# Kernel optimization log

Measured on AMD Instinct MI355X. Metric: run time of the kernel, lower is better.

The kernel has to match this reference:

```python
import jax, jax.numpy as jnp
import numpy as np

HEADS = 8
DIM = 512
DIM_HEAD = DIM // 8        # 64
M = DIM // 2               # 256 landmarks
PINV_ITERS = 6
KERNEL = 33                # residual depthwise conv kernel (33,1)


def moore_penrose_pinv(x, iters):
    # x: [b, h, m, m]; Newton-Schulz style iterative pseudoinverse (lucidrains impl)
    abs_x = jnp.abs(x)
    col = abs_x.sum(axis=-1)
    row = abs_x.sum(axis=-2)
    z = jnp.swapaxes(x, -1, -2) / (jnp.max(col) * jnp.max(row))
    I = jnp.eye(x.shape[-1], dtype=x.dtype)
    for _ in range(iters):
        xz = x @ z
        z = 0.25 * z @ (13.0 * I - xz @ (15.0 * I - xz @ (7.0 * I - xz)))
    return z


def setup_inputs() -> dict:
    key = jax.random.key(0)
    ks = jax.random.split(key, 5)
    b, n, dim = 4, 8192, DIM
    x = jax.random.normal(ks[0], (b, n, dim), dtype=jnp.float32)
    # to_qkv: Linear(dim, 3*inner_dim, bias=False); inner_dim = heads*dim_head = dim
    w_qkv = jax.random.normal(ks[1], (dim, 3 * dim), dtype=jnp.float32) / np.sqrt(dim)
    # to_out: Linear(inner_dim, dim) with bias (dropout = identity in eval)
    w_out = jax.random.normal(ks[2], (dim, dim), dtype=jnp.float32) / np.sqrt(dim)
    b_out = jax.random.normal(ks[3], (dim,), dtype=jnp.float32) * 0.01
    # res_conv: Conv2d(heads, heads, (33,1), padding=(16,0), groups=heads, bias=False)
    conv_w = jax.random.normal(ks[4], (HEADS, 1, KERNEL, 1), dtype=jnp.float32) / np.sqrt(KERNEL)
    return {"x": x, "w_qkv": w_qkv, "w_out": w_out, "b_out": b_out, "conv_w": conv_w}


def nystrom_attention(x, w_qkv, w_out, b_out, conv_w):
    b, n, dim = x.shape
    h, d, m = HEADS, DIM_HEAD, M
    # pad front so seq len divisible by num_landmarks (no-op for n=8192, m=256)
    pad = (m - n % m) % m
    xp = jnp.pad(x, ((0, 0), (pad, 0), (0, 0)))
    np_ = n + pad

    qkv = xp @ w_qkv                                   # [b, np, 3*dim]
    q, k, v = jnp.split(qkv, 3, axis=-1)
    to_heads = lambda t: t.reshape(b, np_, h, d).transpose(0, 2, 1, 3)  # [b,h,np,d]
    q, k, v = to_heads(q), to_heads(k), to_heads(v)
    q = q * (d ** -0.5)

    l = np_ // m                                       # tokens per landmark
    pool = lambda t: t.reshape(b, h, m, l, d).mean(axis=3)  # [b,h,m,d]
    q_l, k_l = pool(q), pool(k)

    attn1 = jax.nn.softmax(jnp.einsum('bhnd,bhmd->bhnm', q, k_l), axis=-1)    # [b,h,np,m]
    attn2 = jax.nn.softmax(jnp.einsum('bhid,bhjd->bhij', q_l, k_l), axis=-1)  # [b,h,m,m]
    attn3 = jax.nn.softmax(jnp.einsum('bhmd,bhnd->bhmn', q_l, k), axis=-1)    # [b,h,m,np]

    attn2_inv = moore_penrose_pinv(attn2, PINV_ITERS)
    out = (attn1 @ attn2_inv) @ (attn3 @ v)            # [b,h,np,d]

    # depthwise conv residual over the sequence axis, per head
    res = jax.lax.conv_general_dilated(
        v, conv_w, window_strides=(1, 1),
        padding=((KERNEL // 2, KERNEL // 2), (0, 0)),
        dimension_numbers=('NCHW', 'OIHW', 'NCHW'),
        feature_group_count=h)
    out = out + res

    out = out.transpose(0, 2, 1, 3).reshape(b, np_, dim)
    out = out @ w_out + b_out
    return out[:, -n:]


def reference(x, w_qkv, w_out, b_out, conv_w):
    return x + nystrom_attention(x, w_qkv, w_out, b_out, conv_w)
```

## Files before the change

kernel.cpp:

```cpp
#include <hip/hip_runtime.h>


#define N_SEQ 8192
#define DMODEL 512
#define NHEAD 8
#define DHEAD 64
#define NLAND 256
#define BH 32

typedef unsigned short u16;
typedef __attribute__((ext_vector_type(8))) short bh8;
typedef __attribute__((ext_vector_type(4))) float fx4;

__device__ __forceinline__ float bf2f(u16 u) { return __uint_as_float(((unsigned)u) << 16); }
__device__ __forceinline__ u16 f2bf(float f) {
    unsigned x = __float_as_uint(f);
    return (u16)((x + 0x7fffu + ((x >> 16) & 1u)) >> 16);
}
__device__ __forceinline__ fx4 mfma16(bh8 a, bh8 b, fx4 c) {
    return __builtin_amdgcn_mfma_f32_16x16x32_bf16(a, b, c, 0, 0, 0);
}
__device__ __forceinline__ void gload16(u16* lds, const u16* g) {
    __builtin_amdgcn_global_load_lds(
        (const __attribute__((address_space(1))) unsigned int*)g,
        (__attribute__((address_space(3))) unsigned int*)lds, 16, 0, 0);
}

__global__ void detect_kernel(const u16* __restrict__ X, unsigned* flag_out)
{
    __shared__ int cnt;
    if (threadIdx.x == 0) cnt = 0;
    __syncthreads();
    u16 u = X[threadIdx.x * 2];
    int e = (u >> 7) & 0xFF;
    int insane = (u != 0) && (e < 90 || e > 140);
    atomicAdd(&cnt, insane);
    __syncthreads();
    if (threadIdx.x == 0) flag_out[0] = (cnt > 64) ? 1u : 0u;
}

__global__ __launch_bounds__(256) void convert4_kernel(
    const void* __restrict__ in, u16* __restrict__ out, int n4, const unsigned* __restrict__ flag)
{
    int i = blockIdx.x * 256 + threadIdx.x;
    if (i >= n4) return;
    if (flag[0]) {
        float4 v = ((const float4*)in)[i];
        ushort4 o;
        o.x = f2bf(v.x); o.y = f2bf(v.y); o.z = f2bf(v.z); o.w = f2bf(v.w);
        ((ushort4*)out)[i] = o;
    } else {
        ((ushort4*)out)[i] = ((const ushort4*)in)[i];
    }
}

__global__ __launch_bounds__(256) void wtrans_kernel(
    const void* __restrict__ in, u16* __restrict__ out, int rows, int cols,
    const unsigned* __restrict__ flag)
{
    int idx = blockIdx.x * 256 + threadIdx.x;
    if (idx >= rows * cols) return;
    int r = idx / cols, c = idx % cols;
    float v = flag[0] ? ((const float*)in)[idx] : bf2f(((const u16*)in)[idx]);
    out[(size_t)c * rows + r] = f2bf(v);
}

__global__ __launch_bounds__(256) void qkv_mfma_kernel(
    const u16* __restrict__ X, const u16* __restrict__ WT,
    u16* __restrict__ Q, u16* __restrict__ K, u16* __restrict__ VT)
{
    __shared__ u16 Xs[128 * 64];
    __shared__ u16 Ws[128 * 64];
    const int tid = threadIdx.x;
    const int wave = tid >> 6, lane = tid & 63;
    const int wrow = (wave >> 1) * 64, wcol = (wave & 1) * 64;
    const int i0 = blockIdx.x * 128;
    const int j0 = blockIdx.y * 128;
    const int la = lane >> 3, lb = lane & 7;
    const int lm = lane & 15, lq = lane >> 4;
    const int sw = lm & 7;
    const int sc = (lb ^ la) * 8;
    fx4 acc[4][4];
#pragma unroll
    for (int a = 0; a < 4; ++a)
#pragma unroll
        for (int b = 0; b < 4; ++b) acc[a][b] = (fx4){0.f, 0.f, 0.f, 0.f};

    for (int k0 = 0; k0 < DMODEL; k0 += 64) {
        __syncthreads();
#pragma unroll
        for (int jj = 0; jj < 4; ++jj) {
            int rb = wave * 32 + jj * 8;
            gload16(Xs + rb * 64, X + (size_t)(i0 + rb + la) * DMODEL + k0 + sc);
            gload16(Ws + rb * 64, WT + (size_t)(j0 + rb + la) * DMODEL + k0 + sc);
        }
        __syncthreads();
#pragma unroll
        for (int ks = 0; ks < 2; ++ks) {
            const int po = ((ks * 4 + lq) ^ sw) * 8;
            bh8 xf[4], wf[4];
#pragma unroll
            for (int im = 0; im < 4; ++im)
                xf[im] = *(const bh8*)(Xs + (wrow + im * 16 + lm) * 64 + po);
#pragma unroll
            for (int in = 0; in < 4; ++in)
                wf[in] = *(const bh8*)(Ws + (wcol + in * 16 + lm) * 64 + po);
#pragma unroll
            for (int im = 0; im < 4; ++im)
#pragma unroll
                for (int in = 0; in < 4; ++in)
                    acc[im][in] = mfma16(wf[in], xf[im], acc[im][in]);
        }
    }
#pragma unroll
    for (int im = 0; im < 4; ++im) {
        int m = i0 + wrow + im * 16 + lm;
        int bb = m >> 13, ns = m & (N_SEQ - 1);
#pragma unroll
        for (int in = 0; in < 4; ++in) {
            int nn = j0 + wcol + in * 16 + (lq << 2);
            int which = nn >> 9;
            int h = (nn >> 6) & 7;
            int d = nn & 63;
            if (which == 2) {
                size_t vb = (size_t)(bb * NHEAD + h) * DHEAD;
#pragma unroll
                for (int cc = 0; cc < 4; ++cc)
                    VT[(vb + d + cc) * N_SEQ + ns] = f2bf(acc[im][in][cc]);
            } else {
                u16* dst = (which == 0) ? Q : K;
                float s = (which == 0) ? 0.125f : 1.f;
                ushort4 o;
                o.x = f2bf(acc[im][in][0] * s); o.y = f2bf(acc[im][in][1] * s);
                o.z = f2bf(acc[im][in][2] * s); o.w = f2bf(acc[im][in][3] * s);
                *(ushort4*)(dst + ((size_t)(bb * NHEAD + h) * N_SEQ + ns) * DHEAD + d) = o;
            }
        }
    }
}

__global__ __launch_bounds__(64) void pool_kernel(
    const u16* __restrict__ Q, const u16* __restrict__ K,
    float* __restrict__ QL, float* __restrict__ KL,
    u16* __restrict__ QLb, u16* __restrict__ KLb)
{
    int m = blockIdx.x, bh = blockIdx.y, d = threadIdx.x;
    size_t base = ((size_t)bh * N_SEQ + m * 32) * DHEAD + d;
    float sq = 0.f, sk = 0.f;
#pragma unroll
    for (int i = 0; i < 32; ++i) {
        sq += bf2f(Q[base + i * DHEAD]);
        sk += bf2f(K[base + i * DHEAD]);
    }
    size_t ob = ((size_t)bh * NLAND + m) * DHEAD + d;
    sq *= (1.f / 32.f); sk *= (1.f / 32.f);
    QL[ob] = sq; KL[ob] = sk;
    QLb[ob] = f2bf(sq); KLb[ob] = f2bf(sk);
}

__global__ __launch_bounds__(256) void attn2_kernel(
    const float* __restrict__ QL, const float* __restrict__ KL, float* __restrict__ A2)
{
    __shared__ float qrow[64];
    __shared__ float red[256];
    int i = blockIdx.x, bh = blockIdx.y, j = threadIdx.x;
    if (j < 64) qrow[j] = QL[((size_t)bh * NLAND + i) * DHEAD + j];
    __syncthreads();
    const float* kr = KL + ((size_t)bh * NLAND + j) * DHEAD;
    float lg = 0.f;
#pragma unroll
    for (int d = 0; d < 64; ++d) lg += qrow[d] * kr[d];
    red[j] = lg; __syncthreads();
    for (int s = 128; s > 0; s >>= 1) { if (j < s) red[j] = fmaxf(red[j], red[j + s]); __syncthreads(); }
    float mx = red[0]; __syncthreads();
    float p = __expf(lg - mx);
    red[j] = p; __syncthreads();
    for (int s = 128; s > 0; s >>= 1) { if (j < s) red[j] += red[j + s]; __syncthreads(); }
    float sum = red[0];
    A2[((size_t)bh * NLAND + i) * NLAND + j] = p / sum;
}

__global__ void init_scal_kernel(unsigned* scal) { if (threadIdx.x < 2) scal[threadIdx.x] = 0u; }

__global__ __launch_bounds__(256) void absmax_kernel(const float* __restrict__ A2, unsigned* scal)
{
    __shared__ float red[256];
    int bh = blockIdx.x, t = threadIdx.x;
    const float* Ab = A2 + (size_t)bh * 65536;
    float cs = 0.f, rs = 0.f;
    for (int j = 0; j < 256; ++j) cs += fabsf(Ab[t * 256 + j]);
    for (int i = 0; i < 256; ++i) rs += fabsf(Ab[i * 256 + t]);
    red[t] = cs; __syncthreads();
    for (int s = 128; s > 0; s >>= 1) { if (t < s) red[t] = fmaxf(red[t], red[t + s]); __syncthreads(); }
    if (t == 0) atomicMax(scal + 0, __float_as_uint(red[0]));
    __syncthreads();
    red[t] = rs; __syncthreads();
    for (int s = 128; s > 0; s >>= 1) { if (t < s) red[t] = fmaxf(red[t], red[t + s]); __syncthreads(); }
    if (t == 0) atomicMax(scal + 1, __float_as_uint(red[0]));
}

__global__ __launch_bounds__(256) void z0_kernel(
    const float* __restrict__ A2, const unsigned* __restrict__ scal,
    u16* __restrict__ zb, u16* __restrict__ zbT, u16* __restrict__ A2b)
{
    float inv = 1.f / (__uint_as_float(scal[0]) * __uint_as_float(scal[1]));
    size_t idx = (size_t)blockIdx.x * 256 + threadIdx.x;
    size_t bh = idx >> 16;
    int r = (int)(idx & 65535);
    int i = r >> 8, j = r & 255;
    float a = A2[idx];
    zb[idx]  = f2bf(A2[(bh << 16) + (size_t)j * 256 + i] * inv);
    zbT[idx] = f2bf(a * inv);
    A2b[idx] = f2bf(a);
}

__global__ __launch_bounds__(256) void bgemm_mfma_kernel(
    const u16* __restrict__ A, const u16* __restrict__ BT,
    u16* __restrict__ Cn, u16* __restrict__ Ct, const u16* __restrict__ E,
    int N, long sB, long sCn, long sCt, float sc, float alpha, float beta, int wn, int wt)
{
    __shared__ u16 As[64 * 72];
    __shared__ u16 Bs[64 * 72];
    const int tid = threadIdx.x;
    const int wave = tid >> 6, lane = tid & 63;
    const int wm = (wave >> 1) * 32, wnn = (wave & 1) * 32;
    const int i0 = blockIdx.x * 64, j0 = blockIdx.y * 64, bh = blockIdx.z;
    const u16* Ab = A + (size_t)bh * 65536;
    const u16* Bb = BT + (size_t)bh * sB;
    const int srow = tid >> 2, scol = (tid & 3) * 16;
    const int lm = lane & 15, lq = lane >> 4;
    fx4 acc[2][2];
#pragma unroll
    for (int a = 0; a < 2; ++a)
#pragma unroll
        for (int b = 0; b < 2; ++b) acc[a][b] = (fx4){0.f, 0.f, 0.f, 0.f};

    for (int k0 = 0; k0 < 256; k0 += 64) {
        uint4 a0 = *(const uint4*)(Ab + (size_t)(i0 + srow) * 256 + k0 + scol);
        uint4 a1 = *(const uint4*)(Ab + (size_t)(i0 + srow) * 256 + k0 + scol + 8);
        uint4 b0 = *(const uint4*)(Bb + (size_t)(j0 + srow) * 256 + k0 + scol);
        uint4 b1 = *(const uint4*)(Bb + (size_t)(j0 + srow) * 256 + k0 + scol + 8);
        __syncthreads();
        *(uint4*)(As + srow * 72 + scol) = a0;
        *(uint4*)(As + srow * 72 + scol + 8) = a1;
        *(uint4*)(Bs + srow * 72 + scol) = b0;
        *(uint4*)(Bs + srow * 72 + scol + 8) = b1;
        __syncthreads();
#pragma unroll
        for (int ks = 0; ks < 2; ++ks) {
            bh8 lf[2], rf[2];
#pragma unroll
            for (int im = 0; im < 2; ++im)
                lf[im] = *(const bh8*)(As + (wm + im * 16 + lm) * 72 + ks * 32 + lq * 8);
#pragma unroll
            for (int in = 0; in < 2; ++in)
                rf[in] = *(const bh8*)(Bs + (wnn + in * 16 + lm) * 72 + ks * 32 + lq * 8);
#pragma unroll
            for (int im = 0; im < 2; ++im)
#pragma unroll
                for (int in = 0; in < 2; ++in)
                    acc[im][in] = mfma16(lf[im], rf[in], acc[im][in]);
        }
    }
#pragma unroll
    for (int im = 0; im < 2; ++im) {
#pragma unroll
        for (int in = 0; in < 2; ++in) {
            int n = j0 + wnn + in * 16 + lm;
            int m0 = i0 + wm + im * 16 + (lq << 2);
            float c[4];
#pragma unroll
            for (int r = 0; r < 4; ++r) {
                int m = m0 + r;
                float x = beta * acc[im][in][r];
                if (alpha != 0.f)
                    x += alpha * bf2f(E[(size_t)bh * 65536 + (size_t)m * 256 + n]);
                if (m == n) x += sc;
                c[r] = x;
            }
            if (wn) {
#pragma unroll
                for (int r = 0; r < 4; ++r)
                    Cn[(size_t)bh * sCn + (size_t)(m0 + r) * N + n] = f2bf(c[r]);
            }
            if (wt) {
                ushort4 o;
                o.x = f2bf(c[0]); o.y = f2bf(c[1]); o.z = f2bf(c[2]); o.w = f2bf(c[3]);
                *(ushort4*)(Ct + (size_t)bh * sCt + (size_t)n * 256 + m0) = o;
            }
        }
    }
}

__global__ __launch_bounds__(256, 2) void attn3v_mfma_kernel(
    const u16* __restrict__ QLb, const u16* __restrict__ Kb,
    const u16* __restrict__ VTb, u16* __restrict__ PO, float* __restrict__ ML)
{
    __shared__ u16 Ks[64 * 72];
    __shared__ u16 Vs[64 * 72];
    __shared__ u16 Pw[4][64 * 72];
    const int tid = threadIdx.x;
    const int wave = tid >> 6, lane = tid & 63;
    const int q = lane >> 4, l15 = lane & 15;
    const int part = blockIdx.x;
    const int bh = blockIdx.y;
    const int nbase = part * 512;
    const int srow = tid >> 2, scol = (tid & 3) * 16;
    u16* Pp = Pw[wave];
    bh8 qf[4][2];
#pragma unroll
    for (int mt = 0; mt < 4; ++mt)
#pragma unroll
        for (int ks = 0; ks < 2; ++ks)
            qf[mt][ks] = *(const bh8*)(QLb + ((size_t)bh * NLAND + wave * 64 + mt * 16 + l15) * DHEAD + ks * 32 + q * 8);
    float M[4] = {-1e30f, -1e30f, -1e30f, -1e30f};
    float L[4] = {0.f, 0.f, 0.f, 0.f};
    fx4 O[4][4];
#pragma unroll
    for (int mt = 0; mt < 4; ++mt)
#pragma unroll
        for (int dt = 0; dt < 4; ++dt) O[mt][dt] = (fx4){0.f, 0.f, 0.f, 0.f};

    for (int c = 0; c < 8; ++c) {
        const int n0 = nbase + c * 64;
        uint4 k0v = *(const uint4*)(Kb + ((size_t)bh * N_SEQ + n0 + srow) * DHEAD + scol);
        uint4 k1v = *(const uint4*)(Kb + ((size_t)bh * N_SEQ + n0 + srow) * DHEAD + scol + 8);
        uint4 v0v = *(const uint4*)(VTb + ((size_t)bh * DHEAD + srow) * N_SEQ + n0 + scol);
        uint4 v1v = *(const uint4*)(VTb + ((size_t)bh * DHEAD + srow) * N_SEQ + n0 + scol + 8);
        __syncthreads();
        *(uint4*)(Ks + srow * 72 + scol) = k0v;
        *(uint4*)(Ks + srow * 72 + scol + 8) = k1v;
        *(uint4*)(Vs + srow * 72 + scol) = v0v;
        *(uint4*)(Vs + srow * 72 + scol + 8) = v1v;
        __syncthreads();
        fx4 S[4][4];
#pragma unroll
        for (int nt = 0; nt < 4; ++nt)
#pragma unroll
            for (int mt = 0; mt < 4; ++mt) S[nt][mt] = (fx4){0.f, 0.f, 0.f, 0.f};
#pragma unroll
        for (int ks = 0; ks < 2; ++ks) {
            bh8 kf[4];
#pragma unroll
            for (int nt = 0; nt < 4; ++nt)
                kf[nt] = *(const bh8*)(Ks + (nt * 16 + l15) * 72 + ks * 32 + q * 8);
#pragma unroll
            for (int nt = 0; nt < 4; ++nt)
#pragma unroll
                for (int mt = 0; mt < 4; ++mt)
                    S[nt][mt] = mfma16(kf[nt], qf[mt][ks], S[nt][mt]);
        }
#pragma unroll
        for (int mt = 0; mt < 4; ++mt) {
            float cm = -1e30f;
#pragma unroll
            for (int nt = 0; nt < 4; ++nt)
#pragma unroll
                for (int r = 0; r < 4; ++r) cm = fmaxf(cm, S[nt][mt][r]);
            cm = fmaxf(cm, __shfl_xor(cm, 16));
            cm = fmaxf(cm, __shfl_xor(cm, 32));
            float Mn = fmaxf(M[mt], cm);
            float al = __expf(M[mt] - Mn);
            M[mt] = Mn;
            L[mt] *= al;
#pragma unroll
            for (int dt = 0; dt < 4; ++dt) {
                O[mt][dt][0] *= al; O[mt][dt][1] *= al;
                O[mt][dt][2] *= al; O[mt][dt][3] *= al;
            }
            float ps = 0.f;
#pragma unroll
            for (int nt = 0; nt < 4; ++nt)
#pragma unroll
                for (int r = 0; r < 4; ++r) {
                    float p = __expf(S[nt][mt][r] - Mn);
                    ps += p;
                    Pp[(mt * 16 + l15) * 72 + nt * 16 + q * 4 + r] = f2bf(p);
                }
            ps += __shfl_xor(ps, 16);
            ps += __shfl_xor(ps, 32);
            L[mt] += ps;
        }
#pragma unroll
        for (int ks = 0; ks < 2; ++ks) {
            bh8 pf[4];
#pragma unroll
            for (int mt = 0; mt < 4; ++mt)
                pf[mt] = *(const bh8*)(Pp + (mt * 16 + l15) * 72 + ks * 32 + q * 8);
#pragma unroll
            for (int dt = 0; dt < 4; ++dt) {
                bh8 vf = *(const bh8*)(Vs + (dt * 16 + l15) * 72 + ks * 32 + q * 8);
#pragma unroll
                for (int mt = 0; mt < 4; ++mt)
                    O[mt][dt] = mfma16(vf, pf[mt], O[mt][dt]);
            }
        }
    }
#pragma unroll
    for (int mt = 0; mt < 4; ++mt) {
        size_t mrow = (size_t)(bh * 16 + part) * NLAND + wave * 64 + mt * 16 + l15;
#pragma unroll
        for (int dt = 0; dt < 4; ++dt) {
            ushort4 o;
            o.x = f2bf(O[mt][dt][0]); o.y = f2bf(O[mt][dt][1]);
            o.z = f2bf(O[mt][dt][2]); o.w = f2bf(O[mt][dt][3]);
            *(ushort4*)(PO + mrow * DHEAD + dt * 16 + q * 4) = o;
        }
        if (q == 0) { ML[mrow * 2] = M[mt]; ML[mrow * 2 + 1] = L[mt]; }
    }
}

__global__ __launch_bounds__(64) void combine_kernel(
    const u16* __restrict__ PO, const float* __restrict__ ML, u16* __restrict__ W3VT)
{
    int m = blockIdx.x, bh = blockIdx.y, d = threadIdx.x;
    float Mg = -1e30f;
#pragma unroll
    for (int p = 0; p < 16; ++p)
        Mg = fmaxf(Mg, ML[((size_t)(bh * 16 + p) * NLAND + m) * 2]);
    float denom = 0.f, o = 0.f;
#pragma unroll
    for (int p = 0; p < 16; ++p) {
        size_t ix = (size_t)(bh * 16 + p) * NLAND + m;
        float w = __expf(ML[ix * 2] - Mg);
        denom += ML[ix * 2 + 1] * w;
        o += bf2f(PO[ix * DHEAD + d]) * w;
    }
    W3VT[((size_t)bh * DHEAD + d) * NLAND + m] = f2bf(o / denom);
}

__global__ __launch_bounds__(256) void conv_kernel(
    const u16* __restrict__ VT, const u16* __restrict__ CW, u16* __restrict__ RT)
{
    __shared__ float vl[2080];
    __shared__ float cws[33];
    const int tid = threadIdx.x;
    const int c0 = blockIdx.x * 2048;
    const int row = blockIdx.y;
    const int h = (row >> 6) & 7;
    const u16* src = VT + (size_t)row * N_SEQ;
    for (int i = tid; i < 2080; i += 256) {
        int gn = c0 - 16 + i;
        vl[i] = (gn >= 0 && gn < N_SEQ) ? bf2f(src[gn]) : 0.f;
    }
    if (tid < 33) cws[tid] = bf2f(CW[h * 33 + tid]);
    __syncthreads();
    float v[40];
    const int base = tid * 8;
#pragma unroll
    for (int i = 0; i < 40; ++i) v[i] = vl[base + i];
    float s[8];
#pragma unroll
    for (int j = 0; j < 8; ++j) {
        float a = 0.f;
#pragma unroll
        for (int t = 0; t < 33; ++t) a += cws[t] * v[j + t];
        s[j] = a;
    }
    u16* dst = RT + (size_t)row * N_SEQ + c0 + base;
    ushort4 o0, o1;
    o0.x = f2bf(s[0]); o0.y = f2bf(s[1]); o0.z = f2bf(s[2]); o0.w = f2bf(s[3]);
    o1.x = f2bf(s[4]); o1.y = f2bf(s[5]); o1.z = f2bf(s[6]); o1.w = f2bf(s[7]);
    *(ushort4*)dst = o0;
    *(ushort4*)(dst + 4) = o1;
}

__global__ __launch_bounds__(256) void outheads_mfma_kernel(
    const u16* __restrict__ Qb, const u16* __restrict__ KLb,
    const u16* __restrict__ WMT, const u16* __restrict__ RT,
    u16* __restrict__ Y)
{
    __shared__ u16 Pl[64 * 264];
    __shared__ float wmax[4][64];
    __shared__ float wsum[4][64];
    const int tid = threadIdx.x;
    const int wave = tid >> 6, lane = tid & 63;
    const int q = lane >> 4, l15 = lane & 15;
    const int bh = blockIdx.y;
    const int bb = bh >> 3, h = bh & 7;
    const int n0 = blockIdx.x * 64;
    fx4 S[4][4];
#pragma unroll
    for (int a = 0; a < 4; ++a)
#pragma unroll
        for (int b = 0; b < 4; ++b) S[a][b] = (fx4){0.f, 0.f, 0.f, 0.f};
#pragma unroll
    for (int ks = 0; ks < 2; ++ks) {
        bh8 qfr[4];
#pragma unroll
        for (int nt = 0; nt < 4; ++nt)
            qfr[nt] = *(const bh8*)(Qb + ((size_t)bh * N_SEQ + n0 + nt * 16 + l15) * DHEAD + ks * 32 + q * 8);
#pragma unroll
        for (int mt = 0; mt < 4; ++mt) {
            bh8 kf = *(const bh8*)(KLb + ((size_t)bh * NLAND + wave * 64 + mt * 16 + l15) * DHEAD + ks * 32 + q * 8);
#pragma unroll
            for (int nt = 0; nt < 4; ++nt)
                S[nt][mt] = mfma16(qfr[nt], kf, S[nt][mt]);
        }
    }
#pragma unroll
    for (int nt = 0; nt < 4; ++nt)
#pragma unroll
        for (int r = 0; r < 4; ++r) {
            float pm = fmaxf(fmaxf(S[nt][0][r], S[nt][1][r]), fmaxf(S[nt][2][r], S[nt][3][r]));
            pm = fmaxf(pm, __shfl_xor(pm, 1));
            pm = fmaxf(pm, __shfl_xor(pm, 2));
            pm = fmaxf(pm, __shfl_xor(pm, 4));
            pm = fmaxf(pm, __shfl_xor(pm, 8));
            if (l15 == 0) wmax[wave][nt * 16 + q * 4 + r] = pm;
        }
    __syncthreads();
#pragma unroll
    for (int nt = 0; nt < 4; ++nt)
#pragma unroll
        for (int r = 0; r < 4; ++r) {
            int nl = nt * 16 + q * 4 + r;
            float Mf = fmaxf(fmaxf(wmax[0][nl], wmax[1][nl]), fmaxf(wmax[2][nl], wmax[3][nl]));
            float ps = 0.f;
#pragma unroll
            for (int mt = 0; mt < 4; ++mt) {
                float p = __expf(S[nt][mt][r] - Mf);
                ps += p;
                Pl[nl * 264 + wave * 64 + mt * 16 + l15] = f2bf(p);
            }
            ps += __shfl_xor(ps, 1);
            ps += __shfl_xor(ps, 2);
            ps += __shfl_xor(ps, 4);
            ps += __shfl_xor(ps, 8);
            if (l15 == 0) wsum[wave][nl] = ps;
        }
    __syncthreads();
    fx4 O[4];
#pragma unroll
    for (int nt = 0; nt < 4; ++nt) O[nt] = (fx4){0.f, 0.f, 0.f, 0.f};
#pragma unroll
    for (int ks = 0; ks < 8; ++ks) {
        bh8 af = *(const bh8*)(WMT + ((size_t)bh * DHEAD + wave * 16 + l15) * NLAND + ks * 32 + q * 8);
#pragma unroll
        for (int nt = 0; nt < 4; ++nt) {
            bh8 pf = *(const bh8*)(Pl + (size_t)(nt * 16 + l15) * 264 + ks * 32 + q * 8);
            O[nt] = mfma16(af, pf, O[nt]);
        }
    }
#pragma unroll
    for (int nt = 0; nt < 4; ++nt) {
        int nl = nt * 16 + l15;
        float inv = 1.f / (wsum[0][nl] + wsum[1][nl] + wsum[2][nl] + wsum[3][nl]);
        int d0 = wave * 16 + (q << 2);
        fx4 v = O[nt];
#pragma unroll
        for (int c = 0; c < 4; ++c)
            v[c] = v[c] * inv + bf2f(RT[(size_t)(bh * DHEAD + d0 + c) * N_SEQ + n0 + nl]);
        ushort4 o;
        o.x = f2bf(v[0]); o.y = f2bf(v[1]); o.z = f2bf(v[2]); o.w = f2bf(v[3]);
        *(ushort4*)(Y + ((size_t)bb * N_SEQ + n0 + nl) * DMODEL + h * DHEAD + d0) = o;
    }
}

__global__ __launch_bounds__(256) void final_mfma_kernel(
    const u16* __restrict__ Y, const u16* __restrict__ WT,
    const u16* __restrict__ Bias, const u16* __restrict__ X, void* __restrict__ Out,
    const unsigned* __restrict__ flag)
{
    __shared__ u16 Xs[128 * 64];
    __shared__ u16 Ws[128 * 64];
    const int tid = threadIdx.x;
    const int wave = tid >> 6, lane = tid & 63;
    const int wrow = (wave >> 1) * 64, wcol = (wave & 1) * 64;
    const int i0 = blockIdx.x * 128;
    const int j0 = blockIdx.y * 128;
    const int la = lane >> 3, lb = lane & 7;
    const int lm = lane & 15, lq = lane >> 4;
    const int sw = lm & 7;
    const int sc = (lb ^ la) * 8;
    const unsigned isf32 = flag[0];
    fx4 acc[4][4];
#pragma unroll
    for (int a = 0; a < 4; ++a)
#pragma unroll
        for (int b = 0; b < 4; ++b) acc[a][b] = (fx4){0.f, 0.f, 0.f, 0.f};

    for (int k0 = 0; k0 < DMODEL; k0 += 64) {
        __syncthreads();
#pragma unroll
        for (int jj = 0; jj < 4; ++jj) {
            int rb = wave * 32 + jj * 8;
            gload16(Xs + rb * 64, Y + (size_t)(i0 + rb + la) * DMODEL + k0 + sc);
            gload16(Ws + rb * 64, WT + (size_t)(j0 + rb + la) * DMODEL + k0 + sc);
        }
        __syncthreads();
#pragma unroll
        for (int ks = 0; ks < 2; ++ks) {
            const int po = ((ks * 4 + lq) ^ sw) * 8;
            bh8 xf[4], wf[4];
#pragma unroll
            for (int im = 0; im < 4; ++im)
                xf[im] = *(const bh8*)(Xs + (wrow + im * 16 + lm) * 64 + po);
#pragma unroll
            for (int in = 0; in < 4; ++in)
                wf[in] = *(const bh8*)(Ws + (wcol + in * 16 + lm) * 64 + po);
#pragma unroll
            for (int im = 0; im < 4; ++im)
#pragma unroll
                for (int in = 0; in < 4; ++in)
                    acc[im][in] = mfma16(wf[in], xf[im], acc[im][in]);
        }
    }
#pragma unroll
    for (int im = 0; im < 4; ++im) {
        int m = i0 + wrow + im * 16 + lm;
#pragma unroll
        for (int in = 0; in < 4; ++in) {
            int nn = j0 + wcol + in * 16 + (lq << 2);
            ushort4 b4 = *(const ushort4*)(Bias + nn);
            ushort4 x4 = *(const ushort4*)(X + (size_t)m * DMODEL + nn);
            float c0 = acc[im][in][0] + bf2f(b4.x) + bf2f(x4.x);
            float c1 = acc[im][in][1] + bf2f(b4.y) + bf2f(x4.y);
            float c2 = acc[im][in][2] + bf2f(b4.z) + bf2f(x4.z);
            float c3 = acc[im][in][3] + bf2f(b4.w) + bf2f(x4.w);
            if (isf32) {
                *(float4*)((float*)Out + (size_t)m * DMODEL + nn) = make_float4(c0, c1, c2, c3);
            } else {
                ushort4 o;
                o.x = f2bf(c0); o.y = f2bf(c1); o.z = f2bf(c2); o.w = f2bf(c3);
                *(ushort4*)((u16*)Out + (size_t)m * DMODEL + nn) = o;
            }
        }
    }
}

extern "C" void kernel_launch(void* const* d_in, const int* in_sizes, int n_in,
                              void* d_out, int out_size, void* d_ws, size_t ws_size,
                              hipStream_t stream)
{
    (void)in_sizes; (void)n_in; (void)out_size; (void)ws_size;
    char* ws = (char*)d_ws;
    u16*   Xc    = (u16*)(ws + 0);
    u16*   WqkvT = (u16*)(ws + 33554432);
    u16*   WoutT = (u16*)(ws + 35127296);
    u16*   Boutc = (u16*)(ws + 35651584);
    u16*   CWc   = (u16*)(ws + 35652608);
    u16*   Qb    = (u16*)(ws + 35653632);
    u16*   Kb    = (u16*)(ws + 69208064);
    u16*   RT    = (u16*)(ws + 69208064);
    u16*   VTb   = (u16*)(ws + 102762496);
    float* QL    = (float*)(ws + 136316928);
    float* KL    = (float*)(ws + 138414080);
    u16*   QLb   = (u16*)(ws + 140511232);
    u16*   KLb   = (u16*)(ws + 141559808);
    u16*   W3VT  = (u16*)(ws + 142608384);
    u16*   WMT   = (u16*)(ws + 143656960);
    u16*   A2b   = (u16*)(ws + 144705536);
    u16*   zA    = (u16*)(ws + 148899840);
    u16*   zAT   = (u16*)(ws + 153094144);
    float* A2    = (float*)(ws + 157288448);
    u16*   PO    = (u16*)(ws + 157288448);
    float* ML    = (float*)(ws + 174065664);
    u16*   zB    = (u16*)(ws + 165677056);
    u16*   zBT   = (u16*)(ws + 169871360);
    u16*   xz    = (u16*)(ws + 174065664);
    u16*   xzT   = (u16*)(ws + 178259968);
    u16*   t2T   = (u16*)(ws + 182454272);
    u16*   t3T   = (u16*)(ws + 186648576);
    u16*   Yb    = (u16*)(ws + 157288448);
    unsigned* SCAL = (unsigned*)(ws + 190842880);

    detect_kernel<<<1, 256, 0, stream>>>((const u16*)d_in[0], SCAL + 2);
    convert4_kernel<<<16384, 256, 0, stream>>>(d_in[0], Xc, 4194304, SCAL + 2);
    wtrans_kernel<<<3072, 256, 0, stream>>>(d_in[1], WqkvT, 512, 1536, SCAL + 2);
    wtrans_kernel<<<1024, 256, 0, stream>>>(d_in[2], WoutT, 512, 512, SCAL + 2);
    convert4_kernel<<<1, 256, 0, stream>>>(d_in[3], Boutc, 128, SCAL + 2);
    convert4_kernel<<<1, 256, 0, stream>>>(d_in[4], CWc, 66, SCAL + 2);

    qkv_mfma_kernel<<<dim3(256, 12), 256, 0, stream>>>(Xc, WqkvT, Qb, Kb, VTb);
    pool_kernel<<<dim3(256, BH), 64, 0, stream>>>(Qb, Kb, QL, KL, QLb, KLb);
    attn2_kernel<<<dim3(256, BH), 256, 0, stream>>>(QL, KL, A2);
    init_scal_kernel<<<1, 64, 0, stream>>>(SCAL);
    absmax_kernel<<<32, 256, 0, stream>>>(A2, SCAL);
    z0_kernel<<<8192, 256, 0, stream>>>(A2, SCAL, zA, zAT, A2b);

    attn3v_mfma_kernel<<<dim3(16, BH), 256, 0, stream>>>(QLb, Kb, VTb, PO, ML);
    combine_kernel<<<dim3(256, BH), 64, 0, stream>>>(PO, ML, W3VT);
    conv_kernel<<<dim3(4, 2048), 256, 0, stream>>>(VTb, CWc, RT);

    u16 *z = zA, *zT = zAT, *zn = zB, *znT = zBT;
    for (int it = 0; it < 6; ++it) {
        bgemm_mfma_kernel<<<dim3(4, 4, 32), 256, 0, stream>>>(
            A2b, zT, xz, xzT, A2b, 256, 65536, 65536, 65536, 0.f, 0.f, 1.f, 1, 1);
        bgemm_mfma_kernel<<<dim3(4, 4, 32), 256, 0, stream>>>(
            xz, xzT, xz, t2T, xz, 256, 65536, 65536, 65536, 15.f, -7.f, 1.f, 0, 1);
        bgemm_mfma_kernel<<<dim3(4, 4, 32), 256, 0, stream>>>(
            xz, t2T, xz, t3T, xz, 256, 65536, 65536, 65536, 13.f, 0.f, -1.f, 0, 1);
        bgemm_mfma_kernel<<<dim3(4, 4, 32), 256, 0, stream>>>(
            z, t3T, zn, znT, xz, 256, 65536, 65536, 65536, 0.f, 0.f, 0.25f, 1, 1);
        u16* t;
        t = z; z = zn; zn = t;
        t = zT; zT = znT; znT = t;
    }
    bgemm_mfma_kernel<<<dim3(4, 1, 32), 256, 0, stream>>>(
        z, W3VT, WMT, WMT, xz, 64, 16384, 16384, 16384, 0.f, 0.f, 1.f, 0, 1);
    outheads_mfma_kernel<<<dim3(128, BH), 256, 0, stream>>>(Qb, KLb, WMT, RT, Yb);
    final_mfma_kernel<<<dim3(256, 4), 256, 0, stream>>>(Yb, WoutT, Boutc, Xc, d_out, SCAL + 2);
}
```

Measured before the change: 732.5 us.

## Give each wave full landmark rows in outheads kernel to drop block syncs

The outheads kernel now has each wave own 16 query rows across all 256 landmarks, instead of splitting landmarks across waves. The softmax max and sum can then be reduced within a wave, which removes the cross-wave LDS reductions and both __syncthreads. The second MFMA swaps operand roles so the residual read is a vectorized ushort4 load, and launch bounds request 4 blocks per SIMD. In exchange each wave reads all of KL and WMT itself, and the output stores become scalar 2-byte writes.

```diff
diff --git a/kernel.cpp b/kernel.cpp
--- a/kernel.cpp
+++ b/kernel.cpp
@@ -465,95 +465,87 @@
     *(ushort4*)(dst + 4) = o1;
 }
 
-__global__ __launch_bounds__(256) void outheads_mfma_kernel(
+__global__ __launch_bounds__(256, 4) void outheads_mfma_kernel(
     const u16* __restrict__ Qb, const u16* __restrict__ KLb,
     const u16* __restrict__ WMT, const u16* __restrict__ RT,
     u16* __restrict__ Y)
 {
-    __shared__ u16 Pl[64 * 264];
-    __shared__ float wmax[4][64];
-    __shared__ float wsum[4][64];
+    __shared__ u16 Pl[4][16 * 264];
     const int tid = threadIdx.x;
     const int wave = tid >> 6, lane = tid & 63;
     const int q = lane >> 4, l15 = lane & 15;
     const int bh = blockIdx.y;
     const int bb = bh >> 3, h = bh & 7;
-    const int n0 = blockIdx.x * 64;
-    fx4 S[4][4];
-#pragma unroll
-    for (int a = 0; a < 4; ++a)
-#pragma unroll
-        for (int b = 0; b < 4; ++b) S[a][b] = (fx4){0.f, 0.f, 0.f, 0.f};
-#pragma unroll
-    for (int ks = 0; ks < 2; ++ks) {
-        bh8 qfr[4];
-#pragma unroll
-        for (int nt = 0; nt < 4; ++nt)
-            qfr[nt] = *(const bh8*)(Qb + ((size_t)bh * N_SEQ + n0 + nt * 16 + l15) * DHEAD + ks * 32 + q * 8);
-#pragma unroll
-        for (int mt = 0; mt < 4; ++mt) {
-            bh8 kf = *(const bh8*)(KLb + ((size_t)bh * NLAND + wave * 64 + mt * 16 + l15) * DHEAD + ks * 32 + q * 8);
-#pragma unroll
-            for (int nt = 0; nt < 4; ++nt)
-                S[nt][mt] = mfma16(qfr[nt], kf, S[nt][mt]);
-        }
-    }
-#pragma unroll
-    for (int nt = 0; nt < 4; ++nt)
+    const int n0 = blockIdx.x * 64 + wave * 16;
+    u16* Pp = Pl[wave];
+
+    bh8 qA[2];
+#pragma unroll
+    for (int ks = 0; ks < 2; ++ks)
+        qA[ks] = *(const bh8*)(Qb + ((size_t)bh * N_SEQ + n0 + l15) * DHEAD + ks * 32 + q * 8);
+
+    fx4 S[16];
+#pragma unroll
+    for (int mt = 0; mt < 16; ++mt) S[mt] = (fx4){0.f, 0.f, 0.f, 0.f};
+    const u16* KLp = KLb + (size_t)bh * NLAND * DHEAD;
+#pragma unroll
+    for (int mt = 0; mt < 16; ++mt) {
+        bh8 k0 = *(const bh8*)(KLp + (size_t)(mt * 16 + l15) * DHEAD + q * 8);
+        bh8 k1 = *(const bh8*)(KLp + (size_t)(mt * 16 + l15) * DHEAD + 32 + q * 8);
+        S[mt] = mfma16(qA[0], k0, S[mt]);
+        S[mt] = mfma16(qA[1], k1, S[mt]);
+    }
+
+    float L[4];
+#pragma unroll
+    for (int r = 0; r < 4; ++r) {
+        float m = S[0][r];
+#pragma unroll
+        for (int mt = 1; mt < 16; ++mt) m = fmaxf(m, S[mt][r]);
+        m = fmaxf(m, __shfl_xor(m, 1));
+        m = fmaxf(m, __shfl_xor(m, 2));
+        m = fmaxf(m, __shfl_xor(m, 4));
+        m = fmaxf(m, __shfl_xor(m, 8));
+        float s = 0.f;
+#pragma unroll
+        for (int mt = 0; mt < 16; ++mt) {
+            float p = __expf(S[mt][r] - m);
+            s += p;
+            Pp[(q * 4 + r) * 264 + mt * 16 + l15] = f2bf(p);
+        }
+        s += __shfl_xor(s, 1);
+        s += __shfl_xor(s, 2);
+        s += __shfl_xor(s, 4);
+        s += __shfl_xor(s, 8);
+        L[r] = s;
+    }
+
+    fx4 O[4];
+#pragma unroll
+    for (int dt = 0; dt < 4; ++dt) O[dt] = (fx4){0.f, 0.f, 0.f, 0.f};
+    const u16* WMp = WMT + (size_t)bh * DHEAD * NLAND;
+#pragma unroll
+    for (int ks = 0; ks < 8; ++ks) {
+        bh8 pf = *(const bh8*)(Pp + l15 * 264 + ks * 32 + q * 8);
+#pragma unroll
+        for (int dt = 0; dt < 4; ++dt) {
+            bh8 wf = *(const bh8*)(WMp + (size_t)(dt * 16 + l15) * NLAND + ks * 32 + q * 8);
+            O[dt] = mfma16(pf, wf, O[dt]);
+        }
+    }
+
+    float inv[4];
+#pragma unroll
+    for (int r = 0; r < 4; ++r) inv[r] = 1.f / L[r];
+#pragma unroll
+    for (int dt = 0; dt < 4; ++dt) {
+        ushort4 rt4 = *(const ushort4*)(RT + ((size_t)bh * DHEAD + dt * 16 + l15) * N_SEQ + n0 + q * 4);
+        const u16* rp = (const u16*)&rt4;
 #pragma unroll
         for (int r = 0; r < 4; ++r) {
-            float pm = fmaxf(fmaxf(S[nt][0][r], S[nt][1][r]), fmaxf(S[nt][2][r], S[nt][3][r]));
-            pm = fmaxf(pm, __shfl_xor(pm, 1));
-            pm = fmaxf(pm, __shfl_xor(pm, 2));
-            pm = fmaxf(pm, __shfl_xor(pm, 4));
-            pm = fmaxf(pm, __shfl_xor(pm, 8));
-            if (l15 == 0) wmax[wave][nt * 16 + q * 4 + r] = pm;
-        }
-    __syncthreads();
-#pragma unroll
-    for (int nt = 0; nt < 4; ++nt)
-#pragma unroll
-        for (int r = 0; r < 4; ++r) {
-            int nl = nt * 16 + q * 4 + r;
-            float Mf = fmaxf(fmaxf(wmax[0][nl], wmax[1][nl]), fmaxf(wmax[2][nl], wmax[3][nl]));
-            float ps = 0.f;
-#pragma unroll
-            for (int mt = 0; mt < 4; ++mt) {
-                float p = __expf(S[nt][mt][r] - Mf);
-                ps += p;
-                Pl[nl * 264 + wave * 64 + mt * 16 + l15] = f2bf(p);
-            }
-            ps += __shfl_xor(ps, 1);
-            ps += __shfl_xor(ps, 2);
-            ps += __shfl_xor(ps, 4);
-            ps += __shfl_xor(ps, 8);
-            if (l15 == 0) wsum[wave][nl] = ps;
-        }
-    __syncthreads();
-    fx4 O[4];
-#pragma unroll
-    for (int nt = 0; nt < 4; ++nt) O[nt] = (fx4){0.f, 0.f, 0.f, 0.f};
-#pragma unroll
-    for (int ks = 0; ks < 8; ++ks) {
-        bh8 af = *(const bh8*)(WMT + ((size_t)bh * DHEAD + wave * 16 + l15) * NLAND + ks * 32 + q * 8);
-#pragma unroll
-        for (int nt = 0; nt < 4; ++nt) {
-            bh8 pf = *(const bh8*)(Pl + (size_t)(nt * 16 + l15) * 264 + ks * 32 + q * 8);
-            O[nt] = mfma16(af, pf, O[nt]);
-        }
-    }
-#pragma unroll
-    for (int nt = 0; nt < 4; ++nt) {
-        int nl = nt * 16 + l15;
-        float inv = 1.f / (wsum[0][nl] + wsum[1][nl] + wsum[2][nl] + wsum[3][nl]);
-        int d0 = wave * 16 + (q << 2);
-        fx4 v = O[nt];
-#pragma unroll
-        for (int c = 0; c < 4; ++c)
-            v[c] = v[c] * inv + bf2f(RT[(size_t)(bh * DHEAD + d0 + c) * N_SEQ + n0 + nl]);
-        ushort4 o;
-        o.x = f2bf(v[0]); o.y = f2bf(v[1]); o.z = f2bf(v[2]); o.w = f2bf(v[3]);
-        *(ushort4*)(Y + ((size_t)bb * N_SEQ + n0 + nl) * DMODEL + h * DHEAD + d0) = o;
+            float v = O[dt][r] * inv[r] + bf2f(rp[r]);
+            Y[((size_t)bb * N_SEQ + n0 + q * 4 + r) * DMODEL + h * DHEAD + dt * 16 + l15] = f2bf(v);
+        }
     }
 }
 
```

New measurement: 764.0 us. +4.3%, slower.

## Fuse pinv iteration GEMMs into one persistent kernel with grid barriers

Applied to the files above, without the earlier changes.

Replaces the 25 separate batched-GEMM launches of the Newton-Schulz pseudoinverse with a single persistent 256-block kernel. Each block computes two 64x64 tiles per stage and synchronises with the other blocks through an atomic-counter grid barrier. The aim is to remove per-launch overhead and idle gaps between small dependent launches. This depends on all 256 blocks being co-resident, or the barrier deadlocks. It also adds spin-wait atomics on one global counter.

```diff
diff --git a/kernel.cpp b/kernel.cpp
--- a/kernel.cpp
+++ b/kernel.cpp
@@ -180,7 +180,11 @@
     A2[((size_t)bh * NLAND + i) * NLAND + j] = p / sum;
 }
 
-__global__ void init_scal_kernel(unsigned* scal) { if (threadIdx.x < 2) scal[threadIdx.x] = 0u; }
+__global__ void init_scal_kernel(unsigned* scal)
+{
+    if (threadIdx.x < 2) scal[threadIdx.x] = 0u;
+    if (threadIdx.x == 2) scal[3] = 0u;
+}
 
 __global__ __launch_bounds__(256) void absmax_kernel(const float* __restrict__ A2, unsigned* scal)
 {
@@ -214,17 +218,17 @@
     A2b[idx] = f2bf(a);
 }
 
-__global__ __launch_bounds__(256) void bgemm_mfma_kernel(
+__device__ __forceinline__ void bgemm_tile(
+    u16* As, u16* Bs,
     const u16* __restrict__ A, const u16* __restrict__ BT,
     u16* __restrict__ Cn, u16* __restrict__ Ct, const u16* __restrict__ E,
-    int N, long sB, long sCn, long sCt, float sc, float alpha, float beta, int wn, int wt)
-{
-    __shared__ u16 As[64 * 72];
-    __shared__ u16 Bs[64 * 72];
+    int N, long sB, long sCn, long sCt,
+    float sc, float alpha, float beta, int wn, int wt,
+    int i0, int j0, int bh)
+{
     const int tid = threadIdx.x;
     const int wave = tid >> 6, lane = tid & 63;
     const int wm = (wave >> 1) * 32, wnn = (wave & 1) * 32;
-    const int i0 = blockIdx.x * 64, j0 = blockIdx.y * 64, bh = blockIdx.z;
     const u16* Ab = A + (size_t)bh * 65536;
     const u16* Bb = BT + (size_t)bh * sB;
     const int srow = tid >> 2, scol = (tid & 3) * 16;
@@ -289,6 +293,74 @@
                 *(ushort4*)(Ct + (size_t)bh * sCt + (size_t)n * 256 + m0) = o;
             }
         }
+    }
+}
+
+__device__ __forceinline__ void gsync(unsigned* bar, unsigned* phase)
+{
+    __syncthreads();
+    if (threadIdx.x == 0) {
+        __threadfence();
+        unsigned ph = ++(*phase);
+        atomicAdd(bar, 1u);
+        while (atomicAdd(bar, 0u) < ph * 256u) {}
+        __threadfence();
+    }
+    __syncthreads();
+}
+
+__global__ __launch_bounds__(256, 2) void pinv_sync_kernel(
+    const u16* __restrict__ A2b,
+    u16* zA, u16* zAT, u16* zB, u16* zBT,
+    u16* xz, u16* xzT, u16* t2T, u16* t3T,
+    const u16* __restrict__ W3VT, u16* __restrict__ WMT,
+    unsigned* bar)
+{
+    __shared__ u16 As[64 * 72];
+    __shared__ u16 Bs[64 * 72];
+    const int bid = blockIdx.x;
+    const int bh = bid >> 3;
+    const int tt0 = (bid & 7) * 2;
+    unsigned phase = 0;
+    u16 *z = zA, *zT = zAT, *zn = zB, *znT = zBT;
+#pragma unroll 1
+    for (int it = 0; it < 6; ++it) {
+#pragma unroll 1
+        for (int t = 0; t < 2; ++t) {
+            const int tt = tt0 + t, i0 = (tt >> 2) * 64, j0 = (tt & 3) * 64;
+            bgemm_tile(As, Bs, A2b, zT, xz, xzT, A2b, 256, 65536, 65536, 65536,
+                       0.f, 0.f, 1.f, 1, 1, i0, j0, bh);
+        }
+        gsync(bar, &phase);
+#pragma unroll 1
+        for (int t = 0; t < 2; ++t) {
+            const int tt = tt0 + t, i0 = (tt >> 2) * 64, j0 = (tt & 3) * 64;
+            bgemm_tile(As, Bs, xz, xzT, xz, t2T, xz, 256, 65536, 65536, 65536,
+                       15.f, -7.f, 1.f, 0, 1, i0, j0, bh);
+        }
+        gsync(bar, &phase);
+#pragma unroll 1
+        for (int t = 0; t < 2; ++t) {
+            const int tt = tt0 + t, i0 = (tt >> 2) * 64, j0 = (tt & 3) * 64;
+            bgemm_tile(As, Bs, xz, t2T, xz, t3T, xz, 256, 65536, 65536, 65536,
+                       13.f, 0.f, -1.f, 0, 1, i0, j0, bh);
+        }
+        gsync(bar, &phase);
+#pragma unroll 1
+        for (int t = 0; t < 2; ++t) {
+            const int tt = tt0 + t, i0 = (tt >> 2) * 64, j0 = (tt & 3) * 64;
+            bgemm_tile(As, Bs, z, t3T, zn, znT, xz, 256, 65536, 65536, 65536,
+                       0.f, 0.f, 0.25f, 1, 1, i0, j0, bh);
+        }
+        gsync(bar, &phase);
+        u16* tp;
+        tp = z;  z = zn;   zn = tp;
+        tp = zT; zT = znT; znT = tp;
+    }
+    if (bid < 128) {
+        const int fh = bid >> 2, fi = (bid & 3) * 64;
+        bgemm_tile(As, Bs, z, W3VT, WMT, WMT, A2b, 64, 16384, 16384, 16384,
+                   0.f, 0.f, 1.f, 0, 1, fi, 0, fh);
     }
 }
 
@@ -683,22 +755,9 @@
     combine_kernel<<<dim3(256, BH), 64, 0, stream>>>(PO, ML, W3VT);
     conv_kernel<<<dim3(4, 2048), 256, 0, stream>>>(VTb, CWc, RT);
 
-    u16 *z = zA, *zT = zAT, *zn = zB, *znT = zBT;
-    for (int it = 0; it < 6; ++it) {
-        bgemm_mfma_kernel<<<dim3(4, 4, 32), 256, 0, stream>>>(
-            A2b, zT, xz, xzT, A2b, 256, 65536, 65536, 65536, 0.f, 0.f, 1.f, 1, 1);
-        bgemm_mfma_kernel<<<dim3(4, 4, 32), 256, 0, stream>>>(
-            xz, xzT, xz, t2T, xz, 256, 65536, 65536, 65536, 15.f, -7.f, 1.f, 0, 1);
-        bgemm_mfma_kernel<<<dim3(4, 4, 32), 256, 0, stream>>>(
-            xz, t2T, xz, t3T, xz, 256, 65536, 65536, 65536, 13.f, 0.f, -1.f, 0, 1);
-        bgemm_mfma_kernel<<<dim3(4, 4, 32), 256, 0, stream>>>(
-            z, t3T, zn, znT, xz, 256, 65536, 65536, 65536, 0.f, 0.f, 0.25f, 1, 1);
-        u16* t;
-        t = z; z = zn; zn = t;
-        t = zT; zT = znT; znT = t;
-    }
-    bgemm_mfma_kernel<<<dim3(4, 1, 32), 256, 0, stream>>>(
-        z, W3VT, WMT, WMT, xz, 64, 16384, 16384, 16384, 0.f, 0.f, 1.f, 0, 1);
+    pinv_sync_kernel<<<256, 256, 0, stream>>>(
+        A2b, zA, zAT, zB, zBT, xz, xzT, t2T, t3T, W3VT, WMT, SCAL + 3);
+
     outheads_mfma_kernel<<<dim3(128, BH), 256, 0, stream>>>(Qb, KLb, WMT, RT, Yb);
     final_mfma_kernel<<<dim3(256, 4), 256, 0, stream>>>(Yb, WoutT, Boutc, Xc, d_out, SCAL + 2);
 }
```

Result: slower. 1.367 ms (+86.6%).

## Restructure pinv iteration to update xz via paired GEMM and prefetch all K tiles

Applied to the files above, without the earlier changes.

The Newton-Schulz loop now carries u = x·z across iterations. Each step computes z_new = 0.25·z·T and u_new = 0.25·u·T in one paired launch over a doubled grid, instead of recomputing x·z in a separate GEMM. This cuts per-iteration launches from four to three. It also raises parallelism for the last GEMM, at the cost of a slightly different rounding path in bf16. Separately, the batched GEMM now loads all four K chunks into registers up front rather than loading each inside the loop, which raises register use but hides global latency.

```diff
diff --git a/kernel.cpp b/kernel.cpp
--- a/kernel.cpp
+++ b/kernel.cpp
@@ -229,22 +229,30 @@
     const u16* Bb = BT + (size_t)bh * sB;
     const int srow = tid >> 2, scol = (tid & 3) * 16;
     const int lm = lane & 15, lq = lane >> 4;
+
+    uint4 ra[4][2], rb[4][2];
+#pragma unroll
+    for (int kc = 0; kc < 4; ++kc) {
+        const u16* ap = Ab + (size_t)(i0 + srow) * 256 + kc * 64 + scol;
+        const u16* bp = Bb + (size_t)(j0 + srow) * 256 + kc * 64 + scol;
+        ra[kc][0] = *(const uint4*)(ap);
+        ra[kc][1] = *(const uint4*)(ap + 8);
+        rb[kc][0] = *(const uint4*)(bp);
+        rb[kc][1] = *(const uint4*)(bp + 8);
+    }
     fx4 acc[2][2];
 #pragma unroll
     for (int a = 0; a < 2; ++a)
 #pragma unroll
         for (int b = 0; b < 2; ++b) acc[a][b] = (fx4){0.f, 0.f, 0.f, 0.f};
 
-    for (int k0 = 0; k0 < 256; k0 += 64) {
-        uint4 a0 = *(const uint4*)(Ab + (size_t)(i0 + srow) * 256 + k0 + scol);
-        uint4 a1 = *(const uint4*)(Ab + (size_t)(i0 + srow) * 256 + k0 + scol + 8);
-        uint4 b0 = *(const uint4*)(Bb + (size_t)(j0 + srow) * 256 + k0 + scol);
-        uint4 b1 = *(const uint4*)(Bb + (size_t)(j0 + srow) * 256 + k0 + scol + 8);
-        __syncthreads();
-        *(uint4*)(As + srow * 72 + scol) = a0;
-        *(uint4*)(As + srow * 72 + scol + 8) = a1;
-        *(uint4*)(Bs + srow * 72 + scol) = b0;
-        *(uint4*)(Bs + srow * 72 + scol + 8) = b1;
+#pragma unroll
+    for (int kc = 0; kc < 4; ++kc) {
+        __syncthreads();
+        *(uint4*)(As + srow * 72 + scol) = ra[kc][0];
+        *(uint4*)(As + srow * 72 + scol + 8) = ra[kc][1];
+        *(uint4*)(Bs + srow * 72 + scol) = rb[kc][0];
+        *(uint4*)(Bs + srow * 72 + scol + 8) = rb[kc][1];
         __syncthreads();
 #pragma unroll
         for (int ks = 0; ks < 2; ++ks) {
@@ -287,6 +295,86 @@
                 ushort4 o;
                 o.x = f2bf(c[0]); o.y = f2bf(c[1]); o.z = f2bf(c[2]); o.w = f2bf(c[3]);
                 *(ushort4*)(Ct + (size_t)bh * sCt + (size_t)n * 256 + m0) = o;
+            }
+        }
+    }
+}
+
+__global__ __launch_bounds__(256) void bgemm_pair_kernel(
+    const u16* __restrict__ Az, const u16* __restrict__ Au, const u16* __restrict__ BT,
+    u16* __restrict__ Czn, u16* __restrict__ Cun, u16* __restrict__ CunT)
+{
+    __shared__ u16 As[64 * 72];
+    __shared__ u16 Bs[64 * 72];
+    const int tid = threadIdx.x;
+    const int wave = tid >> 6, lane = tid & 63;
+    const int wm = (wave >> 1) * 32, wnn = (wave & 1) * 32;
+    const int i0 = blockIdx.x * 64, j0 = blockIdx.y * 64;
+    const int bz = blockIdx.z;
+    const int bh = bz & 31;
+    const int isU = bz >> 5;
+    const u16* Ab = (isU ? Au : Az) + (size_t)bh * 65536;
+    const u16* Bb = BT + (size_t)bh * 65536;
+    const int srow = tid >> 2, scol = (tid & 3) * 16;
+    const int lm = lane & 15, lq = lane >> 4;
+
+    uint4 ra[4][2], rb[4][2];
+#pragma unroll
+    for (int kc = 0; kc < 4; ++kc) {
+        const u16* ap = Ab + (size_t)(i0 + srow) * 256 + kc * 64 + scol;
+        const u16* bp = Bb + (size_t)(j0 + srow) * 256 + kc * 64 + scol;
+        ra[kc][0] = *(const uint4*)(ap);
+        ra[kc][1] = *(const uint4*)(ap + 8);
+        rb[kc][0] = *(const uint4*)(bp);
+        rb[kc][1] = *(const uint4*)(bp + 8);
+    }
+    fx4 acc[2][2];
+#pragma unroll
+    for (int a = 0; a < 2; ++a)
+#pragma unroll
+        for (int b = 0; b < 2; ++b) acc[a][b] = (fx4){0.f, 0.f, 0.f, 0.f};
+
+#pragma unroll
+    for (int kc = 0; kc < 4; ++kc) {
+        __syncthreads();
+        *(uint4*)(As + srow * 72 + scol) = ra[kc][0];
+        *(uint4*)(As + srow * 72 + scol + 8) = ra[kc][1];
+        *(uint4*)(Bs + srow * 72 + scol) = rb[kc][0];
+        *(uint4*)(Bs + srow * 72 + scol + 8) = rb[kc][1];
+        __syncthreads();
+#pragma unroll
+        for (int ks = 0; ks < 2; ++ks) {
+            bh8 lf[2], rf[2];
+#pragma unroll
+            for (int im = 0; im < 2; ++im)
+                lf[im] = *(const bh8*)(As + (wm + im * 16 + lm) * 72 + ks * 32 + lq * 8);
+#pragma unroll
+            for (int in = 0; in < 2; ++in)
+                rf[in] = *(const bh8*)(Bs + (wnn + in * 16 + lm) * 72 + ks * 32 + lq * 8);
+#pragma unroll
+            for (int im = 0; im < 2; ++im)
+#pragma unroll
+                for (int in = 0; in < 2; ++in)
+                    acc[im][in] = mfma16(lf[im], rf[in], acc[im][in]);
+        }
+    }
+#pragma unroll
+    for (int im = 0; im < 2; ++im) {
+#pragma unroll
+        for (int in = 0; in < 2; ++in) {
+            int n = j0 + wnn + in * 16 + lm;
+            int m0 = i0 + wm + im * 16 + (lq << 2);
+            float c[4];
+#pragma unroll
+            for (int r = 0; r < 4; ++r) c[r] = 0.25f * acc[im][in][r];
+            u16* rows = isU ? Cun : Czn;
+#pragma unroll
+            for (int r = 0; r < 4; ++r)
+                rows[(size_t)bh * 65536 + (size_t)(m0 + r) * 256 + n] = f2bf(c[r]);
+            if (isU) {
+                ushort4 o;
+                o.x = f2bf(c[0]); o.y = f2bf(c[1]); o.z = f2bf(c[2]); o.w = f2bf(c[3]);
+                *(ushort4*)(CunT + (size_t)bh * 65536 + (size_t)n * 256 + m0) = o;
             }
         }
     }
@@ -683,22 +771,25 @@
     combine_kernel<<<dim3(256, BH), 64, 0, stream>>>(PO, ML, W3VT);
     conv_kernel<<<dim3(4, 2048), 256, 0, stream>>>(VTb, CWc, RT);
 
-    u16 *z = zA, *zT = zAT, *zn = zB, *znT = zBT;
+    u16 *z = zA, *zn = zB;
+    u16 *u = xz, *uT = xzT, *un = zAT, *unT = zBT;
+    bgemm_mfma_kernel<<<dim3(4, 4, 32), 256, 0, stream>>>(
+        A2b, zAT, u, uT, A2b, 256, 65536, 65536, 65536, 0.f, 0.f, 1.f, 1, 1);
     for (int it = 0; it < 6; ++it) {
         bgemm_mfma_kernel<<<dim3(4, 4, 32), 256, 0, stream>>>(
-            A2b, zT, xz, xzT, A2b, 256, 65536, 65536, 65536, 0.f, 0.f, 1.f, 1, 1);
+            u, uT, u, t2T, u, 256, 65536, 65536, 65536, 15.f, -7.f, 1.f, 0, 1);
         bgemm_mfma_kernel<<<dim3(4, 4, 32), 256, 0, stream>>>(
-            xz, xzT, xz, t2T, xz, 256, 65536, 65536, 65536, 15.f, -7.f, 1.f, 0, 1);
-        bgemm_mfma_kernel<<<dim3(4, 4, 32), 256, 0, stream>>>(
-            xz, t2T, xz, t3T, xz, 256, 65536, 65536, 65536, 13.f, 0.f, -1.f, 0, 1);
-        bgemm_mfma_kernel<<<dim3(4, 4, 32), 256, 0, stream>>>(
-            z, t3T, zn, znT, xz, 256, 65536, 65536, 65536, 0.f, 0.f, 0.25f, 1, 1);
-        u16* t;
-        t = z; z = zn; zn = t;
-        t = zT; zT = znT; znT = t;
+            u, t2T, u, t3T, u, 256, 65536, 65536, 65536, 13.f, 0.f, -1.f, 0, 1);
+        bgemm_pair_kernel<<<dim3(4, 4, 64), 256, 0, stream>>>(
+            z, u, t3T, zn, un, unT);
+        u16* tp;
+        tp = z;  z = zn;  zn = tp;
+        tp = u;  u = un;  un = tp;
+        tp = uT; uT = unT; unT = tp;
     }
     bgemm_mfma_kernel<<<dim3(4, 1, 32), 256, 0, stream>>>(
-        z, W3VT, WMT, WMT, xz, 64, 16384, 16384, 16384, 0.f, 0.f, 1.f, 0, 1);
+        z, W3VT, WMT, WMT, A2b, 64, 16384, 16384, 16384, 0.f, 0.f, 1.f, 0, 1);
+
     outheads_mfma_kernel<<<dim3(128, BH), 256, 0, stream>>>(Qb, KLb, WMT, RT, Yb);
     final_mfma_kernel<<<dim3(256, 4), 256, 0, stream>>>(Yb, WoutT, Boutc, Xc, d_out, SCAL + 2);
 }
```

Measured after the change: 1.004 ms. 1.37x slower.
